# Performance work log

Hardware: AMD Instinct MI355X
Metric: run time of the kernel (lower is better)

Reference implementation:

```python
import jax, jax.numpy as jnp
import numpy as np

N = 25000   # nodes
M = 150000  # edges
D = 512     # d_Embedding
H = 8       # heads
DK = 64     # per-head key dim
DV = 64     # per-head value dim


def setup_inputs() -> dict:
    key = jax.random.key(0)
    ks = jax.random.split(key, 8)
    x = jax.random.normal(ks[0], (N, D), jnp.float32)
    edge_index = jax.random.randint(ks[1], (2, M), 0, N).astype(jnp.int32)
    s_in = 1.0 / np.sqrt(D).astype(np.float32)   # fan-in scaling like nn.Linear init
    s_ff = 1.0 / np.sqrt(H * DV).astype(np.float32)
    Wk = jax.random.normal(ks[2], (D, H * DK), jnp.float32) * s_in
    Wq = jax.random.normal(ks[3], (D, H * DK), jnp.float32) * s_in
    Wv = jax.random.normal(ks[4], (D, H * DV), jnp.float32) * s_in
    Wff = jax.random.normal(ks[5], (H * DV, D), jnp.float32) * s_ff
    bk = jnp.zeros((H * DK,), jnp.float32)
    bq = jnp.zeros((H * DK,), jnp.float32)
    bv = jnp.zeros((H * DV,), jnp.float32)
    bff = jnp.zeros((D,), jnp.float32)
    return {"x": x, "edge_index": edge_index, "Wk": Wk, "bk": bk,
            "Wq": Wq, "bq": bq, "Wv": Wv, "bv": bv, "Wff": Wff, "bff": bff}


def reference(x, edge_index, Wk, bk, Wq, bq, Wv, bv, Wff, bff):
    # Q/K/V projections with per-head reshape (make_heads)
    K = (x @ Wk + bk).reshape(-1, H, DK)
    Q = (x @ Wq + bq).reshape(-1, H, DK)
    V = (x @ Wv + bv).reshape(-1, H, DV)
    senders, receivers = edge_index[0], edge_index[1]
    # edge scores: (M, H)
    att = jnp.einsum('mhd,mhd->mh', Q[receivers], K[senders]) / np.sqrt(DK).astype(np.float32)
    att = jnp.exp(att + 3.0 - att.max())  # global-max-shifted exp, as in source
    # normalize by sum of incoming strengths per receiver node (segment softmax denom)
    ssum = jax.ops.segment_sum(att, receivers, num_segments=N)  # (N, H)
    denom = ssum[receivers]
    att = jnp.where(denom == 0, 0.0, att / jnp.where(denom == 0, 1.0, denom))
    # weighted message + scatter-add aggregate: (N, H, DV)
    msg = att[..., None] * V[senders]
    agg = jax.ops.segment_sum(msg, receivers, num_segments=N)
    # aggregate_heads: Linear over concatenated heads
    return agg.reshape(-1, H * DV) @ Wff + bff
```

## Files before the change

### kernel.cpp

```cpp
#include <hip/hip_runtime.h>
#include <hip/hip_bf16.h>

#define DMODEL 512

typedef __attribute__((ext_vector_type(8))) short bf16x8;
typedef __attribute__((ext_vector_type(4))) float f32x4;

__device__ inline void gload_lds16(const void* g, void* s) {
  __builtin_amdgcn_global_load_lds((const __attribute__((address_space(1))) void*)g,
                                   (__attribute__((address_space(3))) void*)s, 16, 0, 0);
}

__device__ inline float bflo(unsigned u) {
  union { float f; unsigned u; } c; c.u = u << 16; return c.f;
}
__device__ inline float bfhi(unsigned u) {
  union { float f; unsigned u; } c; c.u = u & 0xffff0000u; return c.f;
}

template <bool OUT_BF16>
__global__ __launch_bounds__(256)
void gemm_bf16(const __hip_bfloat16* __restrict__ A, const __hip_bfloat16* __restrict__ Wt,
               const float* __restrict__ bias, void* __restrict__ Cv, int Mrows, int ncols) {
  __shared__ __align__(16) short sA[16 * 512];
  __shared__ __align__(16) short sB[16 * 512];
  const int t = threadIdx.x;
  const int lane = t & 63;
  const int wid = t >> 6;
  const int wrow = wid >> 1, wcol = wid & 1;
  const int row0 = blockIdx.y * 128;
  const int col0 = blockIdx.x * 128;
  const int l15 = lane & 15, lq = lane >> 4;

  f32x4 acc[4][4] = {};

  for (int k0 = 0; k0 < DMODEL; k0 += 64) {
#pragma unroll
    for (int j = 0; j < 4; ++j) {
      int i = wid * 4 + j;
      int mt = i & 7, s = i >> 3;
      int ak = k0 + s * 32 + lq * 8;
      int arow = row0 + mt * 16 + l15;
      arow = min(arow, Mrows - 1);
      gload_lds16(A + (size_t)arow * DMODEL + ak, &sA[i * 512]);
      int brow = col0 + mt * 16 + l15;
      gload_lds16(Wt + (size_t)brow * DMODEL + ak, &sB[i * 512]);
    }
    __syncthreads();

#pragma unroll
    for (int s = 0; s < 2; ++s) {
      bf16x8 af[4], bfr[4];
#pragma unroll
      for (int m = 0; m < 4; ++m)
        af[m] = *(const bf16x8*)&sA[(s * 8 + wrow * 4 + m) * 512 + lane * 8];
#pragma unroll
      for (int n = 0; n < 4; ++n)
        bfr[n] = *(const bf16x8*)&sB[(s * 8 + wcol * 4 + n) * 512 + lane * 8];
#pragma unroll
      for (int m = 0; m < 4; ++m)
#pragma unroll
        for (int n = 0; n < 4; ++n)
          acc[m][n] = __builtin_amdgcn_mfma_f32_16x16x32_bf16(af[m], bfr[n], acc[m][n], 0, 0, 0);
    }
    __syncthreads();
  }

#pragma unroll
  for (int m = 0; m < 4; ++m) {
#pragma unroll
    for (int n = 0; n < 4; ++n) {
      int col = col0 + wcol * 64 + n * 16 + l15;
      float bv = bias[col];
#pragma unroll
      for (int i = 0; i < 4; ++i) {
        int row = row0 + wrow * 64 + m * 16 + lq * 4 + i;
        if (row < Mrows) {
          float v = acc[m][n][i] + bv;
          if (OUT_BF16)
            ((__hip_bfloat16*)Cv)[(size_t)row * ncols + col] = __float2bfloat16(v);
          else
            ((float*)Cv)[(size_t)row * ncols + col] = v;
        }
      }
    }
  }
}

__global__ void cvt_kernel(const float* __restrict__ src, __hip_bfloat16* __restrict__ dst, int n) {
  int i = (blockIdx.x * 256 + threadIdx.x) * 4;
  if (i < n) {
    float4 v = *(const float4*)(src + i);
    union { ushort4 u; __hip_bfloat16 h[4]; } o;
    o.h[0] = __float2bfloat16(v.x);
    o.h[1] = __float2bfloat16(v.y);
    o.h[2] = __float2bfloat16(v.z);
    o.h[3] = __float2bfloat16(v.w);
    *(ushort4*)(dst + i) = o.u;
  }
}

__global__ __launch_bounds__(256)
void wt_kernel(const float* __restrict__ W0, const float* __restrict__ W1,
               const float* __restrict__ W2, const float* __restrict__ W3,
               __hip_bfloat16* __restrict__ T0, __hip_bfloat16* __restrict__ T1,
               __hip_bfloat16* __restrict__ T2, __hip_bfloat16* __restrict__ T3) {
  const float* W; __hip_bfloat16* T;
  switch (blockIdx.z) {
    case 0: W = W0; T = T0; break;
    case 1: W = W1; T = T1; break;
    case 2: W = W2; T = T2; break;
    default: W = W3; T = T3; break;
  }
  __shared__ float tile[64][65];
  const int kb = blockIdx.y * 64, nb = blockIdx.x * 64;
  const int tx = threadIdx.x & 63, ty = threadIdx.x >> 6;
  for (int r = ty; r < 64; r += 4)
    tile[r][tx] = W[(size_t)(kb + r) * DMODEL + nb + tx];
  __syncthreads();
  for (int r = ty; r < 64; r += 4)
    T[(size_t)(nb + r) * DMODEL + kb + tx] = __float2bfloat16(tile[tx][r]);
}

__global__ void bias_kernel(const float* __restrict__ bk, const float* __restrict__ bq,
                            const float* __restrict__ bv, float* __restrict__ o) {
  int i = blockIdx.x * 256 + threadIdx.x;
  if (i < 512) o[i] = bk[i];
  else if (i < 1024) o[i] = bq[i - 512];
  else if (i < 1536) o[i] = bv[i - 1024];
}

__global__ void hist_kernel(const int* __restrict__ recv, int* __restrict__ deg, int M_) {
  int m = blockIdx.x * 256 + threadIdx.x;
  if (m < M_) atomicAdd(&deg[recv[m]], 1);
}

__global__ __launch_bounds__(256)
void scan_block(const int* __restrict__ deg, int* __restrict__ offs,
                int* __restrict__ bsum, int n) {
  __shared__ int sd[256];
  const int t = threadIdx.x;
  const int base = blockIdx.x * 1024;
  int v[4], s = 0;
#pragma unroll
  for (int j = 0; j < 4; ++j) {
    int idx = base + t * 4 + j;
    v[j] = (idx < n) ? deg[idx] : 0;
    s += v[j];
  }
  sd[t] = s;
  __syncthreads();
  for (int off = 1; off < 256; off <<= 1) {
    int x = (t >= off) ? sd[t - off] : 0;
    __syncthreads();
    sd[t] += x;
    __syncthreads();
  }
  int run = sd[t] - s;
#pragma unroll
  for (int j = 0; j < 4; ++j) {
    int idx = base + t * 4 + j;
    if (idx < n) offs[idx] = run;
    run += v[j];
  }
  if (t == 255) bsum[blockIdx.x] = sd[255];
}

__global__ void scan_mid(const int* __restrict__ bsum, int* __restrict__ bbase,
                         int nb, int* __restrict__ offs, int n) {
  int t = threadIdx.x;
  int x = (t < nb) ? bsum[t] : 0;
  int v = x;
  for (int off = 1; off < 64; off <<= 1) {
    int y = __shfl_up(v, off);
    if (t >= off) v += y;
  }
  if (t < nb) bbase[t] = v - x;
  if (t == nb - 1) offs[n] = v;
}

__global__ void scan_add(int* __restrict__ offs, const int* __restrict__ bbase,
                         int* __restrict__ cursor, int n) {
  int i = blockIdx.x * 256 + threadIdx.x;
  if (i < n) {
    int o = offs[i] + bbase[i >> 10];
    offs[i] = o;
    cursor[i] = o;
  }
}

__global__ void fill_kernel(const int* __restrict__ senders, const int* __restrict__ recv,
                            int* __restrict__ cursor, int* __restrict__ sidx, int M_) {
  int m = blockIdx.x * 256 + threadIdx.x;
  if (m < M_) {
    int pos = atomicAdd(&cursor[recv[m]], 1);
    sidx[pos] = senders[m];
  }
}

__global__ __launch_bounds__(256)
void attn_kernel(const __hip_bfloat16* __restrict__ QKV, const int* __restrict__ sidx,
                 const int* __restrict__ offs, __hip_bfloat16* __restrict__ agg, int n) {
  const int lane = threadIdx.x & 63;
  const int wid  = threadIdx.x >> 6;
  const int r = blockIdx.x * 4 + wid;
  if (r >= n) return;
  const int start = offs[r];
  const int end   = offs[r + 1];

  uint4 qr = *(const uint4*)(QKV + (size_t)r * 1536 + 512 + lane * 8);
  float q[8] = {bflo(qr.x), bfhi(qr.x), bflo(qr.y), bfhi(qr.y),
                bflo(qr.z), bfhi(qr.z), bflo(qr.w), bfhi(qr.w)};

  float ssum = 0.f;
  float acc[8] = {};
  int e = start;
  for (; e + 2 <= end; e += 2) {
    int s0 = sidx[e], s1 = sidx[e + 1];
    const __hip_bfloat16* p0 = QKV + (size_t)s0 * 1536 + lane * 8;
    const __hip_bfloat16* p1 = QKV + (size_t)s1 * 1536 + lane * 8;
    uint4 k0 = *(const uint4*)p0;
    uint4 v0 = *(const uint4*)(p0 + 1024);
    uint4 k1 = *(const uint4*)p1;
    uint4 v1 = *(const uint4*)(p1 + 1024);
    float d0 = q[0] * bflo(k0.x) + q[1] * bfhi(k0.x) + q[2] * bflo(k0.y) + q[3] * bfhi(k0.y)
             + q[4] * bflo(k0.z) + q[5] * bfhi(k0.z) + q[6] * bflo(k0.w) + q[7] * bfhi(k0.w);
    float d1 = q[0] * bflo(k1.x) + q[1] * bfhi(k1.x) + q[2] * bflo(k1.y) + q[3] * bfhi(k1.y)
             + q[4] * bflo(k1.z) + q[5] * bfhi(k1.z) + q[6] * bflo(k1.w) + q[7] * bfhi(k1.w);
    d0 += __shfl_xor(d0, 1); d1 += __shfl_xor(d1, 1);
    d0 += __shfl_xor(d0, 2); d1 += __shfl_xor(d1, 2);
    d0 += __shfl_xor(d0, 4); d1 += __shfl_xor(d1, 4);
    float w0 = expf(d0 * 0.125f), w1 = expf(d1 * 0.125f);
    ssum += w0 + w1;
    acc[0] += w0 * bflo(v0.x) + w1 * bflo(v1.x);
    acc[1] += w0 * bfhi(v0.x) + w1 * bfhi(v1.x);
    acc[2] += w0 * bflo(v0.y) + w1 * bflo(v1.y);
    acc[3] += w0 * bfhi(v0.y) + w1 * bfhi(v1.y);
    acc[4] += w0 * bflo(v0.z) + w1 * bflo(v1.z);
    acc[5] += w0 * bfhi(v0.z) + w1 * bfhi(v1.z);
    acc[6] += w0 * bflo(v0.w) + w1 * bflo(v1.w);
    acc[7] += w0 * bfhi(v0.w) + w1 * bfhi(v1.w);
  }
  if (e < end) {
    int s0 = sidx[e];
    const __hip_bfloat16* p0 = QKV + (size_t)s0 * 1536 + lane * 8;
    uint4 k0 = *(const uint4*)p0;
    uint4 v0 = *(const uint4*)(p0 + 1024);
    float d0 = q[0] * bflo(k0.x) + q[1] * bfhi(k0.x) + q[2] * bflo(k0.y) + q[3] * bfhi(k0.y)
             + q[4] * bflo(k0.z) + q[5] * bfhi(k0.z) + q[6] * bflo(k0.w) + q[7] * bfhi(k0.w);
    d0 += __shfl_xor(d0, 1);
    d0 += __shfl_xor(d0, 2);
    d0 += __shfl_xor(d0, 4);
    float w0 = expf(d0 * 0.125f);
    ssum += w0;
    acc[0] += w0 * bflo(v0.x); acc[1] += w0 * bfhi(v0.x);
    acc[2] += w0 * bflo(v0.y); acc[3] += w0 * bfhi(v0.y);
    acc[4] += w0 * bflo(v0.z); acc[5] += w0 * bfhi(v0.z);
    acc[6] += w0 * bflo(v0.w); acc[7] += w0 * bfhi(v0.w);
  }
  const float inv = (end > start) ? 1.0f / ssum : 0.f;
  union { ushort4 u; __hip_bfloat16 h[4]; } o0, o1;
  o0.h[0] = __float2bfloat16(acc[0] * inv); o0.h[1] = __float2bfloat16(acc[1] * inv);
  o0.h[2] = __float2bfloat16(acc[2] * inv); o0.h[3] = __float2bfloat16(acc[3] * inv);
  o1.h[0] = __float2bfloat16(acc[4] * inv); o1.h[1] = __float2bfloat16(acc[5] * inv);
  o1.h[2] = __float2bfloat16(acc[6] * inv); o1.h[3] = __float2bfloat16(acc[7] * inv);
  *(ushort4*)(agg + (size_t)r * DMODEL + lane * 8)     = o0.u;
  *(ushort4*)(agg + (size_t)r * DMODEL + lane * 8 + 4) = o1.u;
}

extern "C" void kernel_launch(void* const* d_in, const int* in_sizes, int n_in,
                              void* d_out, int out_size, void* d_ws, size_t ws_size,
                              hipStream_t stream) {
  const float* x    = (const float*)d_in[0];
  const int*   eidx = (const int*)d_in[1];
  const float* Wk   = (const float*)d_in[2];
  const float* bk   = (const float*)d_in[3];
  const float* Wq   = (const float*)d_in[4];
  const float* bq   = (const float*)d_in[5];
  const float* Wv   = (const float*)d_in[6];
  const float* bv   = (const float*)d_in[7];
  const float* Wff  = (const float*)d_in[8];
  const float* bff  = (const float*)d_in[9];
  float* out = (float*)d_out;

  const int N_ = in_sizes[0] / DMODEL;
  const int M_ = in_sizes[1] / 2;
  const int* senders = eidx;
  const int* recv    = eidx + M_;

  __hip_bfloat16* QKVb = (__hip_bfloat16*)d_ws;
  __hip_bfloat16* xb   = QKVb + (size_t)N_ * 1536;
  __hip_bfloat16* aggb = xb + (size_t)N_ * DMODEL;
  __hip_bfloat16* WtQKV = aggb + (size_t)N_ * DMODEL;
  __hip_bfloat16* Wtff  = WtQKV + 3 * DMODEL * DMODEL;
  float* bqkv = (float*)(Wtff + DMODEL * DMODEL);
  int* deg    = (int*)(bqkv + 1536);
  int* offs   = deg + N_;
  int* cursor = offs + N_ + 1;
  int* sidx   = cursor + N_;
  int* bsum   = sidx + M_;
  int* bbase  = bsum + 64;

  const int nblk = (N_ + 1023) / 1024;

  int nx = N_ * DMODEL;
  cvt_kernel<<<(nx / 4 + 255) / 256, 256, 0, stream>>>(x, xb, nx);
  wt_kernel<<<dim3(8, 8, 4), 256, 0, stream>>>(
      Wk, Wq, Wv, Wff,
      WtQKV, WtQKV + DMODEL * DMODEL, WtQKV + 2 * DMODEL * DMODEL, Wtff);
  bias_kernel<<<6, 256, 0, stream>>>(bk, bq, bv, bqkv);

  hipMemsetAsync(deg, 0, N_ * sizeof(int), stream);
  hist_kernel<<<(M_ + 255) / 256, 256, 0, stream>>>(recv, deg, M_);
  scan_block<<<nblk, 256, 0, stream>>>(deg, offs, bsum, N_);
  scan_mid<<<1, 64, 0, stream>>>(bsum, bbase, nblk, offs, N_);
  scan_add<<<(N_ + 255) / 256, 256, 0, stream>>>(offs, bbase, cursor, N_);
  fill_kernel<<<(M_ + 255) / 256, 256, 0, stream>>>(senders, recv, cursor, sidx, M_);

  gemm_bf16<true><<<dim3(1536 / 128, (N_ + 127) / 128), 256, 0, stream>>>(
      xb, WtQKV, bqkv, QKVb, N_, 1536);

  attn_kernel<<<(N_ + 3) / 4, 256, 0, stream>>>(QKVb, sidx, offs, aggb, N_);

  gemm_bf16<false><<<dim3(DMODEL / 128, (N_ + 127) / 128), 256, 0, stream>>>(
      aggb, Wtff, bff, out, N_, DMODEL);
}
```

Before: 360.8 us.

## Pre-pack operands into MFMA fragment layout and use weight-stationary stripe GEMM

Converts x and the attention output directly into a tiled layout that matches the MFMA A-fragment order, and packs the weights into per-64-column stripes. The new GEMM keeps a whole 64x512 weight stripe resident in LDS (64KB per block) and has each wave stream A fragments straight from global memory with register double-buffering, over a persistent grid. This removes the per-k-step LDS staging of A, the block barriers, and the repeated weight reloads. In exchange, occupancy is limited by the large LDS use, A reuse across column stripes is lost, and padded rows add a little extra work.

```diff
diff --git a/kernel.cpp b/kernel.cpp
--- a/kernel.cpp
+++ b/kernel.cpp
@@ -19,107 +19,124 @@
 }
 
 template <bool OUT_BF16>
-__global__ __launch_bounds__(256)
-void gemm_bf16(const __hip_bfloat16* __restrict__ A, const __hip_bfloat16* __restrict__ Wt,
-               const float* __restrict__ bias, void* __restrict__ Cv, int Mrows, int ncols) {
-  __shared__ __align__(16) short sA[16 * 512];
-  __shared__ __align__(16) short sB[16 * 512];
-  const int t = threadIdx.x;
-  const int lane = t & 63;
-  const int wid = t >> 6;
-  const int wrow = wid >> 1, wcol = wid & 1;
-  const int row0 = blockIdx.y * 128;
-  const int col0 = blockIdx.x * 128;
+__global__ __launch_bounds__(512, 2)
+void gemm_stripe(const __hip_bfloat16* __restrict__ Ap,
+                 const __hip_bfloat16* __restrict__ Wp,
+                 const float* __restrict__ bias, void* __restrict__ Cv,
+                 int Nrows, int ncols, int nquads, int G) {
+  __shared__ __align__(16) short sB[32768];
+  const int tid = threadIdx.x;
+  const int lane = tid & 63, w = tid >> 6;
+  const int g = blockIdx.x, stripe = blockIdx.y;
+  const int col0 = stripe * 64;
+  const __hip_bfloat16* Ws = Wp + (size_t)stripe * 32768;
+
+#pragma unroll
+  for (int i = 0; i < 8; ++i)
+    gload_lds16(Ws + (size_t)(i * 512 + tid) * 8, &sB[(i * 512 + tid) * 8]);
+  __syncthreads();
+
   const int l15 = lane & 15, lq = lane >> 4;
 
-  f32x4 acc[4][4] = {};
-
-  for (int k0 = 0; k0 < DMODEL; k0 += 64) {
-#pragma unroll
-    for (int j = 0; j < 4; ++j) {
-      int i = wid * 4 + j;
-      int mt = i & 7, s = i >> 3;
-      int ak = k0 + s * 32 + lq * 8;
-      int arow = row0 + mt * 16 + l15;
-      arow = min(arow, Mrows - 1);
-      gload_lds16(A + (size_t)arow * DMODEL + ak, &sA[i * 512]);
-      int brow = col0 + mt * 16 + l15;
-      gload_lds16(Wt + (size_t)brow * DMODEL + ak, &sB[i * 512]);
+  for (int q = g * 8 + w; q < nquads; q += G * 8) {
+    f32x4 acc[4][4] = {};
+    const __hip_bfloat16* Abase = Ap + (size_t)q * 32768 + lane * 8;
+    bf16x8 a_cur[4], a_nxt[4];
+#pragma unroll
+    for (int m = 0; m < 4; ++m)
+      a_cur[m] = *(const bf16x8*)(Abase + m * 8192);
+
+#pragma unroll 1
+    for (int c = 0; c < 16; ++c) {
+      if (c < 15) {
+#pragma unroll
+        for (int m = 0; m < 4; ++m)
+          a_nxt[m] = *(const bf16x8*)(Abase + m * 8192 + (c + 1) * 512);
+      }
+#pragma unroll
+      for (int n = 0; n < 4; ++n) {
+        bf16x8 bf = *(const bf16x8*)&sB[((n * 16 + c) * 64 + lane) * 8];
+#pragma unroll
+        for (int m = 0; m < 4; ++m)
+          acc[m][n] = __builtin_amdgcn_mfma_f32_16x16x32_bf16(a_cur[m], bf, acc[m][n], 0, 0, 0);
+      }
+      if (c < 15) {
+#pragma unroll
+        for (int m = 0; m < 4; ++m) a_cur[m] = a_nxt[m];
+      }
     }
-    __syncthreads();
-
-#pragma unroll
-    for (int s = 0; s < 2; ++s) {
-      bf16x8 af[4], bfr[4];
-#pragma unroll
-      for (int m = 0; m < 4; ++m)
-        af[m] = *(const bf16x8*)&sA[(s * 8 + wrow * 4 + m) * 512 + lane * 8];
-#pragma unroll
-      for (int n = 0; n < 4; ++n)
-        bfr[n] = *(const bf16x8*)&sB[(s * 8 + wcol * 4 + n) * 512 + lane * 8];
-#pragma unroll
-      for (int m = 0; m < 4; ++m)
-#pragma unroll
-        for (int n = 0; n < 4; ++n)
-          acc[m][n] = __builtin_amdgcn_mfma_f32_16x16x32_bf16(af[m], bfr[n], acc[m][n], 0, 0, 0);
-    }
-    __syncthreads();
-  }
-
-#pragma unroll
-  for (int m = 0; m < 4; ++m) {
-#pragma unroll
-    for (int n = 0; n < 4; ++n) {
-      int col = col0 + wcol * 64 + n * 16 + l15;
-      float bv = bias[col];
-#pragma unroll
-      for (int i = 0; i < 4; ++i) {
-        int row = row0 + wrow * 64 + m * 16 + lq * 4 + i;
-        if (row < Mrows) {
-          float v = acc[m][n][i] + bv;
-          if (OUT_BF16)
-            ((__hip_bfloat16*)Cv)[(size_t)row * ncols + col] = __float2bfloat16(v);
-          else
-            ((float*)Cv)[(size_t)row * ncols + col] = v;
+
+#pragma unroll
+    for (int m = 0; m < 4; ++m) {
+      int rowb = q * 64 + m * 16;
+#pragma unroll
+      for (int n = 0; n < 4; ++n) {
+        int col = col0 + n * 16 + l15;
+        float bv = bias[col];
+#pragma unroll
+        for (int i = 0; i < 4; ++i) {
+          int row = rowb + lq * 4 + i;
+          if (row < Nrows) {
+            float v = acc[m][n][i] + bv;
+            if (OUT_BF16)
+              ((__hip_bfloat16*)Cv)[(size_t)row * ncols + col] = __float2bfloat16(v);
+            else
+              ((float*)Cv)[(size_t)row * ncols + col] = v;
+          }
         }
       }
     }
   }
 }
 
-__global__ void cvt_kernel(const float* __restrict__ src, __hip_bfloat16* __restrict__ dst, int n) {
-  int i = (blockIdx.x * 256 + threadIdx.x) * 4;
-  if (i < n) {
-    float4 v = *(const float4*)(src + i);
-    union { ushort4 u; __hip_bfloat16 h[4]; } o;
-    o.h[0] = __float2bfloat16(v.x);
-    o.h[1] = __float2bfloat16(v.y);
-    o.h[2] = __float2bfloat16(v.z);
-    o.h[3] = __float2bfloat16(v.w);
-    *(ushort4*)(dst + i) = o.u;
-  }
+__global__ void cvtp_kernel(const float* __restrict__ x, __hip_bfloat16* __restrict__ xp,
+                            int Nrows, int NpadRows) {
+  int tid = blockIdx.x * 256 + threadIdx.x;
+  int r = tid >> 6, kb = tid & 63;
+  if (r >= NpadRows) return;
+  int t = r >> 4, c = kb >> 2, qq = kb & 3, lp = qq * 16 + (r & 15);
+  __hip_bfloat16* dst = xp + (size_t)t * 8192 + c * 512 + lp * 8;
+  union { ushort4 u[2]; __hip_bfloat16 h[8]; } o;
+#pragma unroll
+  for (int j = 0; j < 8; ++j) o.h[j] = __float2bfloat16(0.f);
+  if (r < Nrows) {
+    float4 v0 = *(const float4*)(x + (size_t)r * DMODEL + kb * 8);
+    float4 v1 = *(const float4*)(x + (size_t)r * DMODEL + kb * 8 + 4);
+    o.h[0] = __float2bfloat16(v0.x); o.h[1] = __float2bfloat16(v0.y);
+    o.h[2] = __float2bfloat16(v0.z); o.h[3] = __float2bfloat16(v0.w);
+    o.h[4] = __float2bfloat16(v1.x); o.h[5] = __float2bfloat16(v1.y);
+    o.h[6] = __float2bfloat16(v1.z); o.h[7] = __float2bfloat16(v1.w);
+  }
+  *(ushort4*)dst = o.u[0];
+  *(ushort4*)(dst + 4) = o.u[1];
 }
 
 __global__ __launch_bounds__(256)
-void wt_kernel(const float* __restrict__ W0, const float* __restrict__ W1,
-               const float* __restrict__ W2, const float* __restrict__ W3,
-               __hip_bfloat16* __restrict__ T0, __hip_bfloat16* __restrict__ T1,
-               __hip_bfloat16* __restrict__ T2, __hip_bfloat16* __restrict__ T3) {
-  const float* W; __hip_bfloat16* T;
-  switch (blockIdx.z) {
-    case 0: W = W0; T = T0; break;
-    case 1: W = W1; T = T1; break;
-    case 2: W = W2; T = T2; break;
-    default: W = W3; T = T3; break;
-  }
-  __shared__ float tile[64][65];
-  const int kb = blockIdx.y * 64, nb = blockIdx.x * 64;
-  const int tx = threadIdx.x & 63, ty = threadIdx.x >> 6;
-  for (int r = ty; r < 64; r += 4)
-    tile[r][tx] = W[(size_t)(kb + r) * DMODEL + nb + tx];
+void wp_kernel(const float* __restrict__ Wk, const float* __restrict__ Wq,
+               const float* __restrict__ Wv, const float* __restrict__ Wff,
+               __hip_bfloat16* __restrict__ Wp_qkv, __hip_bfloat16* __restrict__ Wp_ff) {
+  int c = blockIdx.x;
+  int S = blockIdx.y;
+  const float* W; __hip_bfloat16* dst;
+  if (S < 8)       { W = Wk;  dst = Wp_qkv + (size_t)S * 32768; }
+  else if (S < 16) { W = Wq;  dst = Wp_qkv + (size_t)S * 32768; }
+  else if (S < 24) { W = Wv;  dst = Wp_qkv + (size_t)S * 32768; }
+  else             { W = Wff; dst = Wp_ff + (size_t)(S - 24) * 32768; }
+  int colbase = (S & 7) * 64;
+  __shared__ float tile[32][64];
+  for (int idx = threadIdx.x; idx < 2048; idx += 256) {
+    int r = idx >> 6, col = idx & 63;
+    tile[r][col] = W[(size_t)(c * 32 + r) * DMODEL + colbase + col];
+  }
   __syncthreads();
-  for (int r = ty; r < 64; r += 4)
-    T[(size_t)(nb + r) * DMODEL + kb + tx] = __float2bfloat16(tile[tx][r]);
+  int n = threadIdx.x >> 6, l = threadIdx.x & 63;
+  union { ushort4 u[2]; __hip_bfloat16 h[8]; } o;
+#pragma unroll
+  for (int j = 0; j < 8; ++j)
+    o.h[j] = __float2bfloat16(tile[(l >> 4) * 8 + j][n * 16 + (l & 15)]);
+  __hip_bfloat16* p = dst + ((size_t)(n * 16 + c) * 64 + l) * 8;
+  *(ushort4*)p = o.u[0];
+  *(ushort4*)(p + 4) = o.u[1];
 }
 
 __global__ void bias_kernel(const float* __restrict__ bk, const float* __restrict__ bq,
@@ -200,7 +217,7 @@
 
 __global__ __launch_bounds__(256)
 void attn_kernel(const __hip_bfloat16* __restrict__ QKV, const int* __restrict__ sidx,
-                 const int* __restrict__ offs, __hip_bfloat16* __restrict__ agg, int n) {
+                 const int* __restrict__ offs, __hip_bfloat16* __restrict__ aggp, int n) {
   const int lane = threadIdx.x & 63;
   const int wid  = threadIdx.x >> 6;
   const int r = blockIdx.x * 4 + wid;
@@ -259,13 +276,13 @@
     acc[6] += w0 * bflo(v0.w); acc[7] += w0 * bfhi(v0.w);
   }
   const float inv = (end > start) ? 1.0f / ssum : 0.f;
-  union { ushort4 u; __hip_bfloat16 h[4]; } o0, o1;
-  o0.h[0] = __float2bfloat16(acc[0] * inv); o0.h[1] = __float2bfloat16(acc[1] * inv);
-  o0.h[2] = __float2bfloat16(acc[2] * inv); o0.h[3] = __float2bfloat16(acc[3] * inv);
-  o1.h[0] = __float2bfloat16(acc[4] * inv); o1.h[1] = __float2bfloat16(acc[5] * inv);
-  o1.h[2] = __float2bfloat16(acc[6] * inv); o1.h[3] = __float2bfloat16(acc[7] * inv);
-  *(ushort4*)(agg + (size_t)r * DMODEL + lane * 8)     = o0.u;
-  *(ushort4*)(agg + (size_t)r * DMODEL + lane * 8 + 4) = o1.u;
+  union { ushort4 u[2]; __hip_bfloat16 h[8]; } o;
+#pragma unroll
+  for (int j = 0; j < 8; ++j) o.h[j] = __float2bfloat16(acc[j] * inv);
+  int t = r >> 4, c = lane >> 2, qq = lane & 3, lp = qq * 16 + (r & 15);
+  __hip_bfloat16* dst = aggp + (size_t)t * 8192 + c * 512 + lp * 8;
+  *(ushort4*)dst = o.u[0];
+  *(ushort4*)(dst + 4) = o.u[1];
 }
 
 extern "C" void kernel_launch(void* const* d_in, const int* in_sizes, int n_in,
@@ -288,12 +305,16 @@
   const int* senders = eidx;
   const int* recv    = eidx + M_;
 
-  __hip_bfloat16* QKVb = (__hip_bfloat16*)d_ws;
-  __hip_bfloat16* xb   = QKVb + (size_t)N_ * 1536;
-  __hip_bfloat16* aggb = xb + (size_t)N_ * DMODEL;
-  __hip_bfloat16* WtQKV = aggb + (size_t)N_ * DMODEL;
-  __hip_bfloat16* Wtff  = WtQKV + 3 * DMODEL * DMODEL;
-  float* bqkv = (float*)(Wtff + DMODEL * DMODEL);
+  const int T16 = (N_ + 15) / 16;
+  const int Q4  = (T16 + 3) / 4;
+  const int Npad = Q4 * 64;
+
+  __hip_bfloat16* xp    = (__hip_bfloat16*)d_ws;
+  __hip_bfloat16* QKVb  = xp + (size_t)Npad * DMODEL;
+  __hip_bfloat16* aggp  = QKVb + (size_t)N_ * 1536;
+  __hip_bfloat16* Wp_qkv = aggp + (size_t)Npad * DMODEL;
+  __hip_bfloat16* Wp_ff  = Wp_qkv + (size_t)24 * 32768;
+  float* bqkv = (float*)(Wp_ff + (size_t)8 * 32768);
   int* deg    = (int*)(bqkv + 1536);
   int* offs   = deg + N_;
   int* cursor = offs + N_ + 1;
@@ -303,11 +324,8 @@
 
   const int nblk = (N_ + 1023) / 1024;
 
-  int nx = N_ * DMODEL;
-  cvt_kernel<<<(nx / 4 + 255) / 256, 256, 0, stream>>>(x, xb, nx);
-  wt_kernel<<<dim3(8, 8, 4), 256, 0, stream>>>(
-      Wk, Wq, Wv, Wff,
-      WtQKV, WtQKV + DMODEL * DMODEL, WtQKV + 2 * DMODEL * DMODEL, Wtff);
+  cvtp_kernel<<<(Npad * 64 + 255) / 256, 256, 0, stream>>>(x, xp, N_, Npad);
+  wp_kernel<<<dim3(16, 32), 256, 0, stream>>>(Wk, Wq, Wv, Wff, Wp_qkv, Wp_ff);
   bias_kernel<<<6, 256, 0, stream>>>(bk, bq, bv, bqkv);
 
   hipMemsetAsync(deg, 0, N_ * sizeof(int), stream);
@@ -317,11 +335,13 @@
   scan_add<<<(N_ + 255) / 256, 256, 0, stream>>>(offs, bbase, cursor, N_);
   fill_kernel<<<(M_ + 255) / 256, 256, 0, stream>>>(senders, recv, cursor, sidx, M_);
 
-  gemm_bf16<true><<<dim3(1536 / 128, (N_ + 127) / 128), 256, 0, stream>>>(
-      xb, WtQKV, bqkv, QKVb, N_, 1536);
-
-  attn_kernel<<<(N_ + 3) / 4, 256, 0, stream>>>(QKVb, sidx, offs, aggb, N_);
-
-  gemm_bf16<false><<<dim3(DMODEL / 128, (N_ + 127) / 128), 256, 0, stream>>>(
-      aggb, Wtff, bff, out, N_, DMODEL);
-}
+  const int Gq = 21;
+  gemm_stripe<true><<<dim3(Gq, 24), 512, 0, stream>>>(xp, Wp_qkv, bqkv, QKVb,
+                                                      N_, 1536, Q4, Gq);
+
+  attn_kernel<<<(N_ + 3) / 4, 256, 0, stream>>>(QKVb, sidx, offs, aggp, N_);
+
+  const int Go = 63;
+  gemm_stripe<false><<<dim3(Go, 8), 512, 0, stream>>>(aggp, Wp_ff, bff, out,
+                                                      N_, DMODEL, Q4, Go);
+}
```

After: 333.7 us. 7.5% less time.
